# Optimization experiments

Hardware: AMD Instinct MI355X
Metric: run time of the kernel (lower is better)

Reference implementation:

```python
import jax, jax.numpy as jnp
import numpy as np
import math

NUM_HEADS = 8
DIM_Q = 512
DIM_K = 512
DIM_V = 512
EPS = 1e-5


def _layernorm(x, g, b):
    mu = jnp.mean(x, axis=-1, keepdims=True)
    var = jnp.mean(jnp.square(x - mu), axis=-1, keepdims=True)
    return (x - mu) * jax.lax.rsqrt(var + EPS) * g + b


def setup_inputs() -> dict:
    key = jax.random.key(0)
    ks = jax.random.split(key, 16)
    B, Nq, Nk = 8, 1024, 1024
    s_q = 1.0 / math.sqrt(DIM_Q)
    s_v = 1.0 / math.sqrt(DIM_V)
    return {
        "Q": jax.random.normal(ks[0], (B, Nq, DIM_Q), jnp.float32),
        "K": jax.random.normal(ks[1], (B, Nk, DIM_K), jnp.float32),
        "Wq": jax.random.uniform(ks[2], (DIM_Q, DIM_V), jnp.float32, -s_q, s_q),
        "bq": jax.random.uniform(ks[3], (DIM_V,), jnp.float32, -s_q, s_q),
        "Wk": jax.random.uniform(ks[4], (DIM_K, DIM_V), jnp.float32, -s_q, s_q),
        "bk": jax.random.uniform(ks[5], (DIM_V,), jnp.float32, -s_q, s_q),
        "Wv": jax.random.uniform(ks[6], (DIM_K, DIM_V), jnp.float32, -s_q, s_q),
        "bv": jax.random.uniform(ks[7], (DIM_V,), jnp.float32, -s_q, s_q),
        "Wo": jax.random.uniform(ks[8], (DIM_V, DIM_V), jnp.float32, -s_v, s_v),
        "bo": jax.random.uniform(ks[9], (DIM_V,), jnp.float32, -s_v, s_v),
        "g0": jnp.ones((DIM_V,), jnp.float32),
        "b0": jnp.zeros((DIM_V,), jnp.float32),
        "g1": jnp.ones((DIM_V,), jnp.float32),
        "b1": jnp.zeros((DIM_V,), jnp.float32),
        "M": jax.random.randint(ks[10], (B, Nq, Nk), 0, 2, jnp.int32),
    }


def reference(Q, K, Wq, bq, Wk, bk, Wv, bv, Wo, bo, g0, b0, g1, b1, M):
    B, Nq, _ = Q.shape
    Nk = K.shape[1]
    H = NUM_HEADS
    d = DIM_V // H
    # projections
    Qp = Q @ Wq + bq                      # [B,Nq,Dv]
    Kp = K @ Wk + bk                      # [B,Nk,Dv]
    Vp = K @ Wv + bv                      # [B,Nk,Dv]
    # split heads: channel h*d+j -> head h (matches torch split/cat ordering)
    Qh = Qp.reshape(B, Nq, H, d)
    Kh = Kp.reshape(B, Nk, H, d)
    Vh = Vp.reshape(B, Nk, H, d)
    # scores scaled by sqrt(dim_V) (faithful to original, NOT sqrt(head_dim))
    A = jnp.einsum("bqhd,bkhd->bhqk", Qh, Kh) / math.sqrt(DIM_V)
    A = jnp.where(M[:, None, :, :] == 0, -jnp.inf, A)
    A = jax.nn.softmax(A, axis=-1)
    # residual add of the (projected, per-head) query, then merge heads
    O = Qh + jnp.einsum("bhqk,bkhd->bqhd", A, Vh)
    O = O.reshape(B, Nq, DIM_V)
    O = _layernorm(O, g0, b0)
    O = O + jax.nn.relu(O @ Wo + bo)
    O = _layernorm(O, g1, b1)
    return O
```

## Files before the change

kernel.cpp:

```cpp
#include <hip/hip_runtime.h>

typedef unsigned short u16;
typedef unsigned int u32;
typedef unsigned long long u64;
typedef __attribute__((ext_vector_type(8))) short short8;
typedef __attribute__((ext_vector_type(4))) float f32x4;

#define BATCH 8
#define NSEQ 1024
#define DMODEL 512
#define HDIM 64
#define QK_SCALE 0.04419417382415922f
#define SCALE_LOG2E 0.06375871114929199f

#define O_QBF 0ULL
#define O_KBF 8388608ULL
#define O_WB  16777216ULL
#define O_MB  18874368ULL
#define O_QP  19922944ULL
#define O_KP  28311552ULL
#define O_VP  36700160ULL

__device__ __forceinline__ u16 f2bf(float f) {
  u32 u = __float_as_uint(f);
  u = (u + 0x7fffu + ((u >> 16) & 1u)) >> 16;
  return (u16)u;
}
__device__ __forceinline__ float bf2f(u16 s) {
  return __uint_as_float(((u32)s) << 16);
}
__device__ __forceinline__ void gload16(const void* g, void* l) {
  __builtin_amdgcn_global_load_lds((const __attribute__((address_space(1))) void*)g,
                                   (__attribute__((address_space(3))) void*)l, 16, 0, 0);
}

__global__ __launch_bounds__(256) void prep_kernel(
    const float* __restrict__ Q, const float* __restrict__ K,
    const float* __restrict__ Wq, const float* __restrict__ Wk,
    const float* __restrict__ Wv, const float* __restrict__ Wo,
    const int* __restrict__ M,
    u16* __restrict__ Qbf, u16* __restrict__ Kbf, u16* __restrict__ Wb,
    u64* __restrict__ Mb)
{
  __shared__ float lds[64 * 68];
  const int bi = blockIdx.x, t = threadIdx.x;
  if (bi < 4096) {
    const float* src = (bi < 2048) ? Q : K;
    u16* dst = (bi < 2048) ? Qbf : Kbf;
    const int lb = bi & 2047;
    const size_t base = ((size_t)lb * 256 + t) * 8;
    float4 a = *(const float4*)(src + base);
    float4 c = *(const float4*)(src + base + 4);
    short8 o;
    o[0] = (short)f2bf(a.x); o[1] = (short)f2bf(a.y);
    o[2] = (short)f2bf(a.z); o[3] = (short)f2bf(a.w);
    o[4] = (short)f2bf(c.x); o[5] = (short)f2bf(c.y);
    o[6] = (short)f2bf(c.z); o[7] = (short)f2bf(c.w);
    *(short8*)(dst + base) = o;
  } else if (bi < 4352) {
    const int qid = bi - 4096;
    const int w = qid >> 6;
    const int tt = qid & 63;
    const int tr = tt >> 3, tc = tt & 7;
    const float* W = (w == 0) ? Wq : (w == 1) ? Wk : (w == 2) ? Wv : Wo;
#pragma unroll
    for (int j = 0; j < 4; ++j) {
      int vi = j * 256 + t;
      int row = vi >> 4, c4 = vi & 15;
      float4 v = *(const float4*)(W + (size_t)(tr * 64 + row) * 512 + tc * 64 + c4 * 4);
      lds[row * 68 + c4 * 4 + 0] = v.x;
      lds[row * 68 + c4 * 4 + 1] = v.y;
      lds[row * 68 + c4 * 4 + 2] = v.z;
      lds[row * 68 + c4 * 4 + 3] = v.w;
    }
    __syncthreads();
#pragma unroll
    for (int j = 0; j < 2; ++j) {
      int oi = j * 256 + t;
      int nl = oi >> 3, k8 = oi & 7;
      short8 o;
#pragma unroll
      for (int i = 0; i < 8; ++i) o[i] = (short)f2bf(lds[(k8 * 8 + i) * 68 + nl]);
      *(short8*)(Wb + (size_t)w * 262144 + (size_t)(tc * 64 + nl) * 512 + tr * 64 + k8 * 8) = o;
    }
  } else {
    const int pb = bi - 4352;
    const int wv = t >> 6, lane = t & 63;
    for (int i = 0; i < 32; ++i) {
      int widx = pb * 128 + wv * 32 + i;
      int kc = widx & 15;
      int qq = (widx >> 4) & 1023;
      int bb = widx >> 14;
      int mv = M[((size_t)bb * 1024 + qq) * 1024 + kc * 64 + lane];
      u64 bal = __ballot(mv != 0);
      if (lane == 0) Mb[widx] = bal;
    }
  }
}

template<int MODE>
__global__ __launch_bounds__(256) void gemm_bt(
    const u16* __restrict__ Aq, const u16* __restrict__ Ak,
    const u16* __restrict__ Wb,
    const float* __restrict__ b0, const float* __restrict__ b1, const float* __restrict__ b2,
    u16* __restrict__ outp, const u16* __restrict__ resid)
{
  __shared__ __align__(16) char Alds[8192];
  __shared__ __align__(16) char Blds[8192];
  const int tid = threadIdx.x;
  const int wv = tid >> 6, lane = tid & 63;
  const int g16 = lane >> 4, l16 = lane & 15;
  const int wr = wv >> 1, wc = wv & 1;
  const int bx = blockIdx.x, by = blockIdx.y, bz = blockIdx.z;

  const u16* A; const u16* W; const float* bias; u16* out;
  if (MODE == 0) {
    A = (bz == 0) ? Aq : Ak;
    W = Wb + (size_t)bz * 262144;
    bias = (bz == 0) ? b0 : ((bz == 1) ? b1 : b2);
    out = outp + (size_t)bz * 4194304;
  } else {
    A = Aq; W = Wb; bias = b0; out = outp;
  }

  const int m0 = bx * 128, n0 = by * 128;
  f32x4 acc[4][4] = {};

  for (int kt = 0; kt < 16; ++kt) {
    const int k0 = kt * 32;
#pragma unroll
    for (int r = 0; r < 2; ++r) {
      int idx = r * 256 + tid;
      int row = idx >> 2, sl = idx & 3;
      gload16(A + (size_t)(m0 + row) * 512 + k0 + sl * 8, Alds + r * 4096 + wv * 1024);
      gload16(W + (size_t)(n0 + row) * 512 + k0 + sl * 8, Blds + r * 4096 + wv * 1024);
    }
    __syncthreads();
    short8 af[4], bfr[4];
#pragma unroll
    for (int mt = 0; mt < 4; ++mt)
      af[mt] = *(const short8*)(Alds + (wr * 64 + mt * 16 + l16) * 64 + g16 * 16);
#pragma unroll
    for (int nt = 0; nt < 4; ++nt)
      bfr[nt] = *(const short8*)(Blds + (wc * 64 + nt * 16 + l16) * 64 + g16 * 16);
#pragma unroll
    for (int mt = 0; mt < 4; ++mt)
#pragma unroll
      for (int nt = 0; nt < 4; ++nt)
        acc[mt][nt] = __builtin_amdgcn_mfma_f32_16x16x32_bf16(af[mt], bfr[nt], acc[mt][nt], 0, 0, 0);
    __syncthreads();
  }

#pragma unroll
  for (int nt = 0; nt < 4; ++nt) {
    int col = n0 + wc * 64 + nt * 16 + l16;
    float bcol = bias[col];
#pragma unroll
    for (int mt = 0; mt < 4; ++mt) {
#pragma unroll
      for (int r = 0; r < 4; ++r) {
        int row = m0 + wr * 64 + mt * 16 + g16 * 4 + r;
        float v = acc[mt][nt][r] + bcol;
        if (MODE == 1) {
          v = fmaxf(v, 0.f) + bf2f(resid[(size_t)row * 512 + col]);
        }
        out[(size_t)row * 512 + col] = f2bf(v);
      }
    }
  }
}

__global__ __launch_bounds__(256) void attn_kernel(
    const u16* __restrict__ Qp, const u16* __restrict__ Kp, const u16* __restrict__ Vp,
    const u64* __restrict__ Mb, u16* __restrict__ O1)
{
  __shared__ __align__(16) char K_lds[8192];
  __shared__ __align__(16) char VT_lds[8192];
  __shared__ __align__(16) char PT_lds[4][2048];

  const int tid = threadIdx.x;
  const int wv = tid >> 6, lane = tid & 63;
  const int g16 = lane >> 4, l16 = lane & 15;
  const int l7 = l16 & 7;

  const int wg = blockIdx.x;
  const int swz = (wg & 7) * 128 + (wg >> 3);
  const int qt = swz & 15;
  const int h = (swz >> 4) & 7;
  const int b = swz >> 7;
  const int qg = qt * 64;
  const int hb = h * HDIM;
  const size_t batch_row = (size_t)b * NSEQ;

  const int q = qg + wv * 16 + l16;

  short8 b_q[2];
#pragma unroll
  for (int c = 0; c < 2; ++c) {
    short8 raw = *(const short8*)(Qp + (batch_row + q) * DMODEL + hb + c * 32 + g16 * 8);
    short8 sc;
#pragma unroll
    for (int j = 0; j < 8; ++j) sc[j] = (short)f2bf(bf2f((u16)raw[j]) * SCALE_LOG2E);
    b_q[c] = sc;
  }

  float mM = -1e30f, lL = 0.f;
  f32x4 accO[4] = {};
  char* Pw = &PT_lds[wv][0];

  for (int kt = 0; kt < 16; ++kt) {
#pragma unroll
    for (int r = 0; r < 2; ++r) {
      int idx = r * 256 + tid;
      int row = idx >> 3, sl = idx & 7;
      int chunk = sl ^ (row & 7);
      gload16(Kp + (batch_row + kt * 64 + row) * DMODEL + hb + chunk * 8,
              K_lds + r * 4096 + wv * 1024);
    }
    {
      int dv2 = (tid & 31) * 2;
      int kg = tid >> 5;
      short8 slo, shi;
#pragma unroll
      for (int j = 0; j < 8; ++j) {
        u32 u = *(const u32*)(Vp + (batch_row + kt * 64 + kg * 8 + j) * DMODEL + hb + dv2);
        slo[j] = (short)(u & 0xffffu);
        shi[j] = (short)(u >> 16);
      }
      *(short8*)(VT_lds + dv2 * 128 + ((kg ^ (dv2 & 7)) << 4)) = slo;
      *(short8*)(VT_lds + (dv2 + 1) * 128 + ((kg ^ ((dv2 + 1) & 7)) << 4)) = shi;
    }
    __syncthreads();

    f32x4 s_[4];
#pragma unroll
    for (int kf = 0; kf < 4; ++kf) {
      int row = kf * 16 + l16;
      short8 ak0 = *(const short8*)(K_lds + row * 128 + ((g16 ^ l7) << 4));
      short8 ak1 = *(const short8*)(K_lds + row * 128 + (((4 + g16) ^ l7) << 4));
      f32x4 acc = {0.f, 0.f, 0.f, 0.f};
      acc = __builtin_amdgcn_mfma_f32_16x16x32_bf16(ak0, b_q[0], acc, 0, 0, 0);
      acc = __builtin_amdgcn_mfma_f32_16x16x32_bf16(ak1, b_q[1], acc, 0, 0, 0);
      s_[kf] = acc;
    }

    u64 mks = Mb[(batch_row + q) * 16 + kt] >> (g16 * 4);
    float p[4][4];
    float mx = -1e30f;
#pragma unroll
    for (int kf = 0; kf < 4; ++kf) {
      u32 nib = ((u32)(mks >> (kf * 16))) & 15u;
#pragma unroll
      for (int r = 0; r < 4; ++r) {
        float v = ((nib >> r) & 1u) ? s_[kf][r] : -1e30f;
        p[kf][r] = v;
        mx = fmaxf(mx, v);
      }
    }
    mx = fmaxf(mx, __shfl_xor(mx, 16, 64));
    mx = fmaxf(mx, __shfl_xor(mx, 32, 64));
    float nm = fmaxf(mM, mx);
    float corr = __builtin_amdgcn_exp2f(mM - nm);
    mM = nm;
    float sum = 0.f;
#pragma unroll
    for (int kf = 0; kf < 4; ++kf)
#pragma unroll
      for (int r = 0; r < 4; ++r) {
        float e = __builtin_amdgcn_exp2f(p[kf][r] - nm);
        p[kf][r] = e;
        sum += e;
      }
    sum += __shfl_xor(sum, 16, 64);
    sum += __shfl_xor(sum, 32, 64);
    lL = lL * corr + sum;
#pragma unroll
    for (int f = 0; f < 4; ++f) {
      accO[f][0] *= corr; accO[f][1] *= corr; accO[f][2] *= corr; accO[f][3] *= corr;
    }

#pragma unroll
    for (int kf = 0; kf < 4; ++kf) {
      int chunk = kf * 2 + (g16 >> 1);
      int off = l16 * 128 + ((chunk ^ l7) << 4) + (g16 & 1) * 8;
      u64 pk = (u64)f2bf(p[kf][0]) | ((u64)f2bf(p[kf][1]) << 16) |
               ((u64)f2bf(p[kf][2]) << 32) | ((u64)f2bf(p[kf][3]) << 48);
      *(u64*)(Pw + off) = pk;
    }

    short8 b_p[2];
#pragma unroll
    for (int kc = 0; kc < 2; ++kc)
      b_p[kc] = *(const short8*)(Pw + l16 * 128 + (((kc * 4 + g16) ^ l7) << 4));
#pragma unroll
    for (int f = 0; f < 4; ++f) {
      int vrow = f * 16 + l16;
      short8 av0 = *(const short8*)(VT_lds + vrow * 128 + ((g16 ^ l7) << 4));
      short8 av1 = *(const short8*)(VT_lds + vrow * 128 + (((4 + g16) ^ l7) << 4));
      accO[f] = __builtin_amdgcn_mfma_f32_16x16x32_bf16(av0, b_p[0], accO[f], 0, 0, 0);
      accO[f] = __builtin_amdgcn_mfma_f32_16x16x32_bf16(av1, b_p[1], accO[f], 0, 0, 0);
    }
    __syncthreads();
  }

  float inv = 1.0f / fmaxf(lL, 1e-20f);
#pragma unroll
  for (int f = 0; f < 4; ++f) {
    size_t o = (batch_row + q) * DMODEL + hb + f * 16 + g16 * 4;
    u64 qh = *(const u64*)(Qp + o);
    u64 ov = 0;
#pragma unroll
    for (int r = 0; r < 4; ++r) {
      float val = accO[f][r] * inv + bf2f((u16)(qh >> (r * 16)));
      ov |= ((u64)f2bf(val)) << (r * 16);
    }
    *(u64*)(O1 + o) = ov;
  }
}

template<int OUTF>
__global__ __launch_bounds__(256) void ln_kernel(
    const u16* __restrict__ X, const float* __restrict__ g, const float* __restrict__ bb,
    void* __restrict__ outv)
{
  const int tid = threadIdx.x;
  const int wv = tid >> 6, lane = tid & 63;
  const size_t row = (size_t)blockIdx.x * 4 + wv;
  short8 x8 = *(const short8*)(X + row * 512 + lane * 8);
  float xf[8];
  float s = 0.f, s2 = 0.f;
#pragma unroll
  for (int i = 0; i < 8; ++i) {
    xf[i] = bf2f((u16)x8[i]);
    s += xf[i];
    s2 += xf[i] * xf[i];
  }
#pragma unroll
  for (int d = 1; d < 64; d <<= 1) {
    s += __shfl_xor(s, d, 64);
    s2 += __shfl_xor(s2, d, 64);
  }
  float mu = s * (1.f / 512.f);
  float var = s2 * (1.f / 512.f) - mu * mu;
  float rs = rsqrtf(var + 1e-5f);
  float4 ga = *(const float4*)(g + lane * 8);
  float4 gb = *(const float4*)(g + lane * 8 + 4);
  float4 ba = *(const float4*)(bb + lane * 8);
  float4 bc = *(const float4*)(bb + lane * 8 + 4);
  float gv[8] = {ga.x, ga.y, ga.z, ga.w, gb.x, gb.y, gb.z, gb.w};
  float bv[8] = {ba.x, ba.y, ba.z, ba.w, bc.x, bc.y, bc.z, bc.w};
  float y[8];
#pragma unroll
  for (int i = 0; i < 8; ++i) y[i] = (xf[i] - mu) * rs * gv[i] + bv[i];
  if (OUTF) {
    float* o = (float*)outv + row * 512 + lane * 8;
    float4 o1 = {y[0], y[1], y[2], y[3]};
    float4 o2 = {y[4], y[5], y[6], y[7]};
    *(float4*)o = o1;
    *(float4*)(o + 4) = o2;
  } else {
    short8 o;
#pragma unroll
    for (int i = 0; i < 8; ++i) o[i] = (short)f2bf(y[i]);
    *(short8*)((u16*)outv + row * 512 + lane * 8) = o;
  }
}

extern "C" void kernel_launch(void* const* d_in, const int* in_sizes, int n_in,
                              void* d_out, int out_size, void* d_ws, size_t ws_size,
                              hipStream_t stream) {
  (void)in_sizes; (void)n_in; (void)out_size; (void)ws_size;
  const float* Q  = (const float*)d_in[0];
  const float* K  = (const float*)d_in[1];
  const float* Wq = (const float*)d_in[2];
  const float* bq = (const float*)d_in[3];
  const float* Wk = (const float*)d_in[4];
  const float* bk = (const float*)d_in[5];
  const float* Wv = (const float*)d_in[6];
  const float* bv = (const float*)d_in[7];
  const float* Wo = (const float*)d_in[8];
  const float* bo = (const float*)d_in[9];
  const float* g0 = (const float*)d_in[10];
  const float* b0 = (const float*)d_in[11];
  const float* g1 = (const float*)d_in[12];
  const float* b1 = (const float*)d_in[13];
  const int*   M  = (const int*)d_in[14];
  float* out = (float*)d_out;
  char* ws = (char*)d_ws;

  u16* Qbf = (u16*)(ws + O_QBF);
  u16* Kbf = (u16*)(ws + O_KBF);
  u16* Wb  = (u16*)(ws + O_WB);
  u64* Mb  = (u64*)(ws + O_MB);
  u16* Qp  = (u16*)(ws + O_QP);
  u16* Kp  = (u16*)(ws + O_KP);
  u16* Vp  = (u16*)(ws + O_VP);
  u16* O1  = Kbf;
  u16* Xn  = Qp;
  u16* Z   = Qbf;

  prep_kernel<<<5376, 256, 0, stream>>>(Q, K, Wq, Wk, Wv, Wo, M, Qbf, Kbf, Wb, Mb);
  gemm_bt<0><<<dim3(64, 4, 3), 256, 0, stream>>>(Qbf, Kbf, Wb, bq, bk, bv, Qp, nullptr);
  attn_kernel<<<1024, 256, 0, stream>>>(Qp, Kp, Vp, Mb, O1);
  ln_kernel<0><<<2048, 256, 0, stream>>>(O1, g0, b0, (void*)Xn);
  gemm_bt<1><<<dim3(64, 4, 1), 256, 0, stream>>>(Xn, nullptr, Wb + 3 * 262144, bo,
                                                 nullptr, nullptr, Z, Xn);
  ln_kernel<1><<<2048, 256, 0, stream>>>(Z, g1, b1, (void*)out);
}
```

Baseline: 119.2 us.

## Double-buffer attention K/V tiles, use bf16 additive mask bias, lazy softmax rescale

```diff
diff --git a/kernel.cpp b/kernel.cpp
--- a/kernel.cpp
+++ b/kernel.cpp
@@ -5,18 +5,17 @@
 typedef unsigned long long u64;
 typedef __attribute__((ext_vector_type(8))) short short8;
 typedef __attribute__((ext_vector_type(4))) float f32x4;
+typedef __attribute__((ext_vector_type(4))) u32 u32x4;
 
 #define BATCH 8
 #define NSEQ 1024
 #define DMODEL 512
 #define HDIM 64
-#define QK_SCALE 0.04419417382415922f
 #define SCALE_LOG2E 0.06375871114929199f
 
 #define O_QBF 0ULL
 #define O_KBF 8388608ULL
 #define O_WB  16777216ULL
-#define O_MB  18874368ULL
 #define O_QP  19922944ULL
 #define O_KP  28311552ULL
 #define O_VP  36700160ULL
@@ -32,6 +31,11 @@
 __device__ __forceinline__ void gload16(const void* g, void* l) {
   __builtin_amdgcn_global_load_lds((const __attribute__((address_space(1))) void*)g,
                                    (__attribute__((address_space(3))) void*)l, 16, 0, 0);
+}
+__device__ __forceinline__ u32 cvtpk(float a, float b) {
+  u32 r;
+  asm("v_cvt_pk_bf16_f32 %0, %1, %2" : "=v"(r) : "v"(a), "v"(b));
+  return r;
 }
 
 __global__ __launch_bounds__(256) void prep_kernel(
@@ -40,7 +44,7 @@
     const float* __restrict__ Wv, const float* __restrict__ Wo,
     const int* __restrict__ M,
     u16* __restrict__ Qbf, u16* __restrict__ Kbf, u16* __restrict__ Wb,
-    u64* __restrict__ Mb)
+    u16* __restrict__ Mbias)
 {
   __shared__ float lds[64 * 68];
   const int bi = blockIdx.x, t = threadIdx.x;
@@ -85,16 +89,19 @@
     }
   } else {
     const int pb = bi - 4352;
-    const int wv = t >> 6, lane = t & 63;
-    for (int i = 0; i < 32; ++i) {
-      int widx = pb * 128 + wv * 32 + i;
-      int kc = widx & 15;
-      int qq = (widx >> 4) & 1023;
-      int bb = widx >> 14;
-      int mv = M[((size_t)bb * 1024 + qq) * 1024 + kc * 64 + lane];
-      u64 bal = __ballot(mv != 0);
-      if (lane == 0) Mb[widx] = bal;
-    }
+    const size_t idx = ((size_t)pb * 256 + t) * 16;
+    const int4* Ms = (const int4*)(M + idx);
+    int4 m0 = Ms[0], m1 = Ms[1], m2 = Ms[2], m3 = Ms[3];
+    int mv[16] = {m0.x, m0.y, m0.z, m0.w, m1.x, m1.y, m1.z, m1.w,
+                  m2.x, m2.y, m2.z, m2.w, m3.x, m3.y, m3.z, m3.w};
+    short8 o0, o1;
+#pragma unroll
+    for (int i = 0; i < 8; ++i) {
+      o0[i] = mv[i] ? (short)0 : (short)0xC700;
+      o1[i] = mv[8 + i] ? (short)0 : (short)0xC700;
+    }
+    *(short8*)(Mbias + idx) = o0;
+    *(short8*)(Mbias + idx + 8) = o1;
   }
 }
 
@@ -170,12 +177,12 @@
   }
 }
 
-__global__ __launch_bounds__(256) void attn_kernel(
+__global__ __launch_bounds__(256, 4) void attn_kernel(
     const u16* __restrict__ Qp, const u16* __restrict__ Kp, const u16* __restrict__ Vp,
-    const u64* __restrict__ Mb, u16* __restrict__ O1)
+    const u16* __restrict__ Mbias, u16* __restrict__ O1)
 {
-  __shared__ __align__(16) char K_lds[8192];
-  __shared__ __align__(16) char VT_lds[8192];
+  __shared__ __align__(16) char K_lds[2][8192];
+  __shared__ __align__(16) char VT_lds[2][8192];
   __shared__ __align__(16) char PT_lds[4][2048];
 
   const int tid = threadIdx.x;
@@ -193,6 +200,8 @@
   const size_t batch_row = (size_t)b * NSEQ;
 
   const int q = qg + wv * 16 + l16;
+  const int dv2 = (tid & 31) * 2;
+  const int kg = tid >> 5;
 
   short8 b_q[2];
 #pragma unroll
@@ -204,88 +213,117 @@
     b_q[c] = sc;
   }
 
-  float mM = -1e30f, lL = 0.f;
-  f32x4 accO[4] = {};
-  char* Pw = &PT_lds[wv][0];
-
-  for (int kt = 0; kt < 16; ++kt) {
+  const u64* Mq = (const u64*)(Mbias + (batch_row + q) * 1024);
+
+  auto stageK = [&](int kt2, char* dst) {
 #pragma unroll
     for (int r = 0; r < 2; ++r) {
       int idx = r * 256 + tid;
       int row = idx >> 3, sl = idx & 7;
       int chunk = sl ^ (row & 7);
-      gload16(Kp + (batch_row + kt * 64 + row) * DMODEL + hb + chunk * 8,
-              K_lds + r * 4096 + wv * 1024);
-    }
-    {
-      int dv2 = (tid & 31) * 2;
-      int kg = tid >> 5;
-      short8 slo, shi;
-#pragma unroll
-      for (int j = 0; j < 8; ++j) {
-        u32 u = *(const u32*)(Vp + (batch_row + kt * 64 + kg * 8 + j) * DMODEL + hb + dv2);
-        slo[j] = (short)(u & 0xffffu);
-        shi[j] = (short)(u >> 16);
-      }
-      *(short8*)(VT_lds + dv2 * 128 + ((kg ^ (dv2 & 7)) << 4)) = slo;
-      *(short8*)(VT_lds + (dv2 + 1) * 128 + ((kg ^ ((dv2 + 1) & 7)) << 4)) = shi;
-    }
+      gload16(Kp + (batch_row + kt2 * 64 + row) * DMODEL + hb + chunk * 8,
+              dst + r * 4096 + wv * 1024);
+    }
+  };
+  auto loadV = [&](int kt2, u32* vr) {
+#pragma unroll
+    for (int j = 0; j < 8; ++j)
+      vr[j] = *(const u32*)(Vp + (batch_row + kt2 * 64 + kg * 8 + j) * DMODEL + hb + dv2);
+  };
+  auto writeVT = [&](const u32* vr, char* dstv) {
+    u32x4 lo, hi;
+#pragma unroll
+    for (int i = 0; i < 4; ++i) {
+      lo[i] = __builtin_amdgcn_perm(vr[2 * i + 1], vr[2 * i], 0x05040100u);
+      hi[i] = __builtin_amdgcn_perm(vr[2 * i + 1], vr[2 * i], 0x07060302u);
+    }
+    *(u32x4*)(dstv + dv2 * 128 + ((kg ^ (dv2 & 7)) << 4)) = lo;
+    *(u32x4*)(dstv + (dv2 + 1) * 128 + ((kg ^ ((dv2 + 1) & 7)) << 4)) = hi;
+  };
+  auto loadBias = [&](int kt2, u64* bb) {
+#pragma unroll
+    for (int kf = 0; kf < 4; ++kf) bb[kf] = Mq[kt2 * 16 + kf * 4 + g16];
+  };
+
+  float mM = -1e30f, lL = 0.f;
+  f32x4 accO[4] = {};
+  char* Pw = &PT_lds[wv][0];
+
+  u32 vreg[8];
+  u64 bias_cur[4], bias_next[4];
+  stageK(0, &K_lds[0][0]);
+  loadV(0, vreg);
+  loadBias(0, bias_cur);
+  writeVT(vreg, &VT_lds[0][0]);
+  loadV(1, vreg);
+
+  for (int kt = 0; kt < 16; ++kt) {
     __syncthreads();
+    char* Kc = &K_lds[kt & 1][0];
+    char* Vc = &VT_lds[kt & 1][0];
+    if (kt < 15) {
+      writeVT(vreg, &VT_lds[(kt + 1) & 1][0]);
+      stageK(kt + 1, &K_lds[(kt + 1) & 1][0]);
+      loadBias(kt + 1, bias_next);
+    }
+    if (kt < 14) loadV(kt + 2, vreg);
 
     f32x4 s_[4];
 #pragma unroll
     for (int kf = 0; kf < 4; ++kf) {
+      u32 blo = (u32)bias_cur[kf];
+      u32 bhi = (u32)(bias_cur[kf] >> 32);
+      f32x4 acc;
+      acc[0] = __uint_as_float(blo << 16);
+      acc[1] = __uint_as_float(blo & 0xffff0000u);
+      acc[2] = __uint_as_float(bhi << 16);
+      acc[3] = __uint_as_float(bhi & 0xffff0000u);
       int row = kf * 16 + l16;
-      short8 ak0 = *(const short8*)(K_lds + row * 128 + ((g16 ^ l7) << 4));
-      short8 ak1 = *(const short8*)(K_lds + row * 128 + (((4 + g16) ^ l7) << 4));
-      f32x4 acc = {0.f, 0.f, 0.f, 0.f};
+      short8 ak0 = *(const short8*)(Kc + row * 128 + ((g16 ^ l7) << 4));
+      short8 ak1 = *(const short8*)(Kc + row * 128 + (((4 + g16) ^ l7) << 4));
       acc = __builtin_amdgcn_mfma_f32_16x16x32_bf16(ak0, b_q[0], acc, 0, 0, 0);
       acc = __builtin_amdgcn_mfma_f32_16x16x32_bf16(ak1, b_q[1], acc, 0, 0, 0);
       s_[kf] = acc;
     }
 
-    u64 mks = Mb[(batch_row + q) * 16 + kt] >> (g16 * 4);
-    float p[4][4];
     float mx = -1e30f;
 #pragma unroll
-    for (int kf = 0; kf < 4; ++kf) {
-      u32 nib = ((u32)(mks >> (kf * 16))) & 15u;
-#pragma unroll
-      for (int r = 0; r < 4; ++r) {
-        float v = ((nib >> r) & 1u) ? s_[kf][r] : -1e30f;
-        p[kf][r] = v;
-        mx = fmaxf(mx, v);
-      }
-    }
+    for (int kf = 0; kf < 4; ++kf)
+#pragma unroll
+      for (int r = 0; r < 4; ++r) mx = fmaxf(mx, s_[kf][r]);
     mx = fmaxf(mx, __shfl_xor(mx, 16, 64));
     mx = fmaxf(mx, __shfl_xor(mx, 32, 64));
-    float nm = fmaxf(mM, mx);
-    float corr = __builtin_amdgcn_exp2f(mM - nm);
-    mM = nm;
+
+    if (!__all(mx <= mM + 8.0f)) {
+      float nm = fmaxf(mM, mx);
+      float corr = __builtin_amdgcn_exp2f(mM - nm);
+      mM = nm;
+      lL *= corr;
+#pragma unroll
+      for (int f = 0; f < 4; ++f) accO[f] *= corr;
+    }
+
     float sum = 0.f;
+    float p[4][4];
 #pragma unroll
     for (int kf = 0; kf < 4; ++kf)
 #pragma unroll
       for (int r = 0; r < 4; ++r) {
-        float e = __builtin_amdgcn_exp2f(p[kf][r] - nm);
+        float e = __builtin_amdgcn_exp2f(s_[kf][r] - mM);
         p[kf][r] = e;
         sum += e;
       }
     sum += __shfl_xor(sum, 16, 64);
     sum += __shfl_xor(sum, 32, 64);
-    lL = lL * corr + sum;
-#pragma unroll
-    for (int f = 0; f < 4; ++f) {
-      accO[f][0] *= corr; accO[f][1] *= corr; accO[f][2] *= corr; accO[f][3] *= corr;
-    }
+    lL += sum;
 
 #pragma unroll
     for (int kf = 0; kf < 4; ++kf) {
       int chunk = kf * 2 + (g16 >> 1);
       int off = l16 * 128 + ((chunk ^ l7) << 4) + (g16 & 1) * 8;
-      u64 pk = (u64)f2bf(p[kf][0]) | ((u64)f2bf(p[kf][1]) << 16) |
-               ((u64)f2bf(p[kf][2]) << 32) | ((u64)f2bf(p[kf][3]) << 48);
-      *(u64*)(Pw + off) = pk;
+      u32 c0 = cvtpk(p[kf][0], p[kf][1]);
+      u32 c1 = cvtpk(p[kf][2], p[kf][3]);
+      *(u64*)(Pw + off) = (u64)c0 | ((u64)c1 << 32);
     }
 
     short8 b_p[2];
@@ -295,12 +333,16 @@
 #pragma unroll
     for (int f = 0; f < 4; ++f) {
       int vrow = f * 16 + l16;
-      short8 av0 = *(const short8*)(VT_lds + vrow * 128 + ((g16 ^ l7) << 4));
-      short8 av1 = *(const short8*)(VT_lds + vrow * 128 + (((4 + g16) ^ l7) << 4));
+      short8 av0 = *(const short8*)(Vc + vrow * 128 + ((g16 ^ l7) << 4));
+      short8 av1 = *(const short8*)(Vc + vrow * 128 + (((4 + g16) ^ l7) << 4));
       accO[f] = __builtin_amdgcn_mfma_f32_16x16x32_bf16(av0, b_p[0], accO[f], 0, 0, 0);
       accO[f] = __builtin_amdgcn_mfma_f32_16x16x32_bf16(av1, b_p[1], accO[f], 0, 0, 0);
     }
-    __syncthreads();
+
+    if (kt < 15) {
+#pragma unroll
+      for (int kf = 0; kf < 4; ++kf) bias_cur[kf] = bias_next[kf];
+    }
   }
 
   float inv = 1.0f / fmaxf(lL, 1e-20f);
@@ -391,17 +433,17 @@
   u16* Qbf = (u16*)(ws + O_QBF);
   u16* Kbf = (u16*)(ws + O_KBF);
   u16* Wb  = (u16*)(ws + O_WB);
-  u64* Mb  = (u64*)(ws + O_MB);
   u16* Qp  = (u16*)(ws + O_QP);
   u16* Kp  = (u16*)(ws + O_KP);
   u16* Vp  = (u16*)(ws + O_VP);
+  u16* Mbias = (u16*)d_out;
   u16* O1  = Kbf;
   u16* Xn  = Qp;
   u16* Z   = Qbf;
 
-  prep_kernel<<<5376, 256, 0, stream>>>(Q, K, Wq, Wk, Wv, Wo, M, Qbf, Kbf, Wb, Mb);
+  prep_kernel<<<6400, 256, 0, stream>>>(Q, K, Wq, Wk, Wv, Wo, M, Qbf, Kbf, Wb, Mbias);
   gemm_bt<0><<<dim3(64, 4, 3), 256, 0, stream>>>(Qbf, Kbf, Wb, bq, bk, bv, Qp, nullptr);
-  attn_kernel<<<1024, 256, 0, stream>>>(Qp, Kp, Vp, Mb, O1);
+  attn_kernel<<<1024, 256, 0, stream>>>(Qp, Kp, Vp, Mbias, O1);
   ln_kernel<0><<<2048, 256, 0, stream>>>(O1, g0, b0, (void*)Xn);
   gemm_bt<1><<<dim3(64, 4, 1), 256, 0, stream>>>(Xn, nullptr, Wb + 3 * 262144, bo,
                                                  nullptr, nullptr, Z, Xn);
```

New measurement: 118.0 us. Within noise of the previous version (-1.0%).
